# Kernel optimization log

Measured on AMD Instinct MI355X. Metric: run time of the kernel, lower is better.

Reference implementation:

```python
import jax, jax.numpy as jnp
import numpy as np

NEG = -9999.0
PAD_IDX = 0
SOS_IDX = 47


def setup_inputs() -> dict:
    key = jax.random.key(0)
    k1, k2, k3 = jax.random.split(key, 3)
    B, T, S = 1024, 512, 48
    features = jax.random.normal(k1, (B, T, S), dtype=jnp.float32)
    states = jax.random.randint(k2, (B, T), 1, S - 1)  # avoid pad/sos as gold tags
    mask = jnp.ones((B, T), dtype=jnp.float32)
    # transition matrix ~ N(-1, 0.1) with CRF structural constraints (as in __init__)
    transition = -1.0 + 0.1 * jax.random.normal(k3, (S, S), dtype=jnp.float32)
    transition = transition.at[SOS_IDX, :].set(NEG)
    transition = transition.at[:, PAD_IDX].set(NEG)
    transition = transition.at[PAD_IDX, :].set(NEG)
    transition = transition.at[PAD_IDX, PAD_IDX].set(0.0)
    return {"features": features, "states": states, "mask": mask, "transition": transition}


def _numerator(features, states, mask, transition):
    # score of the gold path: sum_t mask_t * (emission_t + transition[y_t, y_{t-1}])
    B = states.shape[0]
    sos_col = jnp.full((B, 1), SOS_IDX, dtype=states.dtype)
    states_ext = jnp.concatenate([sos_col, states], axis=1)  # [B, T+1]
    emis = jnp.take_along_axis(features, states[..., None], axis=2)[..., 0]  # [B, T]
    trans = transition[states_ext[:, 1:], states_ext[:, :-1]]  # [B, T]
    return jnp.sum((emis + trans) * mask, axis=1)  # [B]


def _denominator(features, mask, transition):
    # CRF forward algorithm: log-partition via log-sum-exp scan over time
    B, T, S = features.shape
    init = jnp.full((B, S), NEG, dtype=features.dtype).at[:, SOS_IDX].set(0.0)

    def step(score, xs):
        emis_t, mask_t = xs  # [B, S], [B]
        # new[b, i] = lse_j( score[b, j] + emis[b, i] + transition[i, j] )
        new = jax.nn.logsumexp(
            score[:, None, :] + emis_t[:, :, None] + transition[None, :, :], axis=-1
        )
        m = mask_t[:, None]
        return new * m + score * (1.0 - m), None

    final, _ = jax.lax.scan(
        step, init, (jnp.swapaxes(features, 0, 1), jnp.swapaxes(mask, 0, 1))
    )
    return jax.nn.logsumexp(final, axis=-1)  # [B]


def reference(features, states, mask, transition):
    numer = _numerator(features, states, mask, transition)
    denom = _denominator(features, mask, transition)
    # per-sequence negative log-likelihood (denominator - numerator)
    return denom - numer
```

## Files before the change

### kernel.cpp

```cpp
#include <hip/hip_runtime.h>
#include <math.h>

#define B 1024
#define T 512
#define S 48
#define SOS 47

__device__ __forceinline__ float rdlane1(float v) {
    return __int_as_float(__builtin_amdgcn_readlane(__float_as_int(v), 1));
}

__global__ __launch_bounds__(64)
__attribute__((amdgpu_waves_per_eu(1, 1)))
void crf_fused(const float* __restrict__ feat,
               const int* __restrict__ states,
               const float* __restrict__ mask,
               const float* __restrict__ trans,
               float* __restrict__ out) {
    __shared__ __align__(16) float pbuf[2][64];
    __shared__ unsigned long long mbits[T / 64];
    const int b = blockIdx.x;
    const int lane = threadIdx.x;
    const int elane = (lane < S) ? lane : 0;
    const float* f_b = feat + (size_t)b * T * S;
    const float* m_b = mask + b * T;
    const int* st_b = states + b * T;

    float nsum = 0.f;
#pragma unroll
    for (int k2 = 0; k2 < T / 64; ++k2) {
        const int t = lane + k2 * 64;
        const int st = st_b[t];
        const int pv = (t == 0) ? SOS : st_b[t - 1];
        const float m = m_b[t];
        nsum += (f_b[t * S + st] + trans[st * S + pv]) * m;
        const unsigned long long bal = __ballot(m != 0.f);
        if (lane == 0) mbits[k2] = bal;
    }

    float expT[S];
    {
        const float4* t4 = (const float4*)(trans + elane * S);
#pragma unroll
        for (int j4 = 0; j4 < S / 4; ++j4) {
            const float4 tv = t4[j4];
            expT[4 * j4 + 0] = (lane < S) ? __expf(tv.x) : 0.f;
            expT[4 * j4 + 1] = (lane < S) ? __expf(tv.y) : 0.f;
            expT[4 * j4 + 2] = (lane < S) ? __expf(tv.z) : 0.f;
            expT[4 * j4 + 3] = (lane < S) ? __expf(tv.w) : 0.f;
        }
    }

    float q = (lane == SOS) ? 1.f : 0.f;
    float M = 0.f;
    float r_s = 1.f, l_s = 0.f;
    pbuf[0][lane] = q;

    float ering[2][8];
#pragma unroll
    for (int k = 0; k < 8; ++k)
        ering[0][k] = f_b[k * S + elane];

#pragma unroll 2
    for (int tb = 0; tb < T / 8; ++tb) {
        const int pb = tb & 1;
        const int tn = ((tb + 1) & (T / 8 - 1)) * 8;
#pragma unroll
        for (int k = 0; k < 8; ++k)
            ering[pb ^ 1][k] = f_b[(tn + k) * S + elane];
        const unsigned int mbyte =
            ((const volatile unsigned char*)mbits)[tb];
#pragma unroll
        for (int k = 0; k < 8; ++k) {
            const float emis = ering[pb][k];
            const float er = rdlane1(emis);
            const float F = __expf(emis - er) * r_s;
            const float4* qb = (const float4*)pbuf[k & 1];
            float ax = 0.f, ay = 0.f, az = 0.f, aw = 0.f;
#pragma unroll
            for (int j4 = 0; j4 < S / 4; ++j4) {
                const float4 pv4 = qb[j4];
                ax = fmaf(expT[4 * j4 + 0], pv4.x, ax);
                ay = fmaf(expT[4 * j4 + 1], pv4.y, ay);
                az = fmaf(expT[4 * j4 + 2], pv4.z, az);
                aw = fmaf(expT[4 * j4 + 3], pv4.w, aw);
            }
            const float d = (ax + ay) + (az + aw);
            const float qn = d * F;
            const bool live = ((mbyte >> k) & 1u) != 0u;
            q = live ? qn : q;
            pbuf[(k + 1) & 1][lane] = q;
            M = live ? (M + er + l_s) : M;
            const float dr = rdlane1(d);
            const float nl = __logf(dr);
            const float nr = __builtin_amdgcn_rcpf(dr);
            r_s = live ? nr : r_s;
            l_s = live ? nl : l_s;
        }
    }

    float ps = q;
#pragma unroll
    for (int off = 32; off > 0; off >>= 1) {
        ps += __shfl_xor(ps, off, 64);
        nsum += __shfl_xor(nsum, off, 64);
    }
    if (lane == 0) out[b] = M + __logf(ps) - nsum;
}

extern "C" void kernel_launch(void* const* d_in, const int* in_sizes, int n_in,
                              void* d_out, int out_size, void* d_ws, size_t ws_size,
                              hipStream_t stream) {
    const float* feat   = (const float*)d_in[0];
    const int*   states = (const int*)d_in[1];
    const float* mask   = (const float*)d_in[2];
    const float* trans  = (const float*)d_in[3];
    float* out = (float*)d_out;

    crf_fused<<<dim3(B), dim3(64), 0, stream>>>(feat, states, mask, trans, out);
}
```

Measured before the change: 286.7 us.

## Use fp16 dot2 for CRF recurrence and track normalizer via exponent bookkeeping

The exp-transition matrix and the per-step probability vector in LDS are stored as fp16, and the 48-term matvec uses v_dot2 fdot2 instructions, which halves both the FMA count and the LDS read bytes. Per-step normalization now divides by lane 1's value and accumulates the reciprocal scale as a float mantissa plus an integer exponent, so no log is needed per step. The loop unroll drops from 2 to 1. In exchange, fp16 precision risks accuracy loss in the log-partition over 512 steps.

Result: slower. 310.3 us (+8.2%).

```diff
diff --git a/kernel.cpp b/kernel.cpp
--- a/kernel.cpp
+++ b/kernel.cpp
@@ -5,6 +5,9 @@
 #define T 512
 #define S 48
 #define SOS 47
+
+typedef _Float16 half2v __attribute__((ext_vector_type(2)));
+typedef _Float16 half8v __attribute__((ext_vector_type(8)));
 
 __device__ __forceinline__ float rdlane1(float v) {
     return __int_as_float(__builtin_amdgcn_readlane(__float_as_int(v), 1));
@@ -17,7 +20,7 @@
                const float* __restrict__ mask,
                const float* __restrict__ trans,
                float* __restrict__ out) {
-    __shared__ __align__(16) float pbuf[2][64];
+    __shared__ __align__(16) _Float16 qbuf[2][64];
     __shared__ unsigned long long mbits[T / 64];
     const int b = blockIdx.x;
     const int lane = threadIdx.x;
@@ -38,64 +41,71 @@
         if (lane == 0) mbits[k2] = bal;
     }
 
-    float expT[S];
+    half2v eT[S / 2];
     {
         const float4* t4 = (const float4*)(trans + elane * S);
 #pragma unroll
         for (int j4 = 0; j4 < S / 4; ++j4) {
             const float4 tv = t4[j4];
-            expT[4 * j4 + 0] = (lane < S) ? __expf(tv.x) : 0.f;
-            expT[4 * j4 + 1] = (lane < S) ? __expf(tv.y) : 0.f;
-            expT[4 * j4 + 2] = (lane < S) ? __expf(tv.z) : 0.f;
-            expT[4 * j4 + 3] = (lane < S) ? __expf(tv.w) : 0.f;
+            const float e0 = (lane < S) ? __expf(tv.x) : 0.f;
+            const float e1 = (lane < S) ? __expf(tv.y) : 0.f;
+            const float e2 = (lane < S) ? __expf(tv.z) : 0.f;
+            const float e3 = (lane < S) ? __expf(tv.w) : 0.f;
+            eT[2 * j4 + 0] = half2v{(_Float16)e0, (_Float16)e1};
+            eT[2 * j4 + 1] = half2v{(_Float16)e2, (_Float16)e3};
         }
     }
 
     float q = (lane == SOS) ? 1.f : 0.f;
-    float M = 0.f;
-    float r_s = 1.f, l_s = 0.f;
-    pbuf[0][lane] = q;
+    qbuf[0][lane] = (_Float16)q;
+    float P = 1.f;
+    int cexp = 0;
 
     float ering[2][8];
 #pragma unroll
     for (int k = 0; k < 8; ++k)
         ering[0][k] = f_b[k * S + elane];
 
-#pragma unroll 2
+#pragma unroll 1
     for (int tb = 0; tb < T / 8; ++tb) {
-        const int pb = tb & 1;
+        const int pbk = tb & 1;
         const int tn = ((tb + 1) & (T / 8 - 1)) * 8;
 #pragma unroll
         for (int k = 0; k < 8; ++k)
-            ering[pb ^ 1][k] = f_b[(tn + k) * S + elane];
+            ering[pbk ^ 1][k] = f_b[(tn + k) * S + elane];
         const unsigned int mbyte =
             ((const volatile unsigned char*)mbits)[tb];
 #pragma unroll
         for (int k = 0; k < 8; ++k) {
-            const float emis = ering[pb][k];
-            const float er = rdlane1(emis);
-            const float F = __expf(emis - er) * r_s;
-            const float4* qb = (const float4*)pbuf[k & 1];
+            asm volatile("" ::: "memory");
+            const float E = __expf(ering[pbk][k]);
+            const half8v* qb = (const half8v*)&qbuf[k & 1][0];
             float ax = 0.f, ay = 0.f, az = 0.f, aw = 0.f;
 #pragma unroll
-            for (int j4 = 0; j4 < S / 4; ++j4) {
-                const float4 pv4 = qb[j4];
-                ax = fmaf(expT[4 * j4 + 0], pv4.x, ax);
-                ay = fmaf(expT[4 * j4 + 1], pv4.y, ay);
-                az = fmaf(expT[4 * j4 + 2], pv4.z, az);
-                aw = fmaf(expT[4 * j4 + 3], pv4.w, aw);
+            for (int c = 0; c < 6; ++c) {
+                const half8v h = qb[c];
+                const half2v p0 = __builtin_shufflevector(h, h, 0, 1);
+                const half2v p1 = __builtin_shufflevector(h, h, 2, 3);
+                const half2v p2 = __builtin_shufflevector(h, h, 4, 5);
+                const half2v p3 = __builtin_shufflevector(h, h, 6, 7);
+                ax = __builtin_amdgcn_fdot2(eT[4 * c + 0], p0, ax, false);
+                ay = __builtin_amdgcn_fdot2(eT[4 * c + 1], p1, ay, false);
+                az = __builtin_amdgcn_fdot2(eT[4 * c + 2], p2, az, false);
+                aw = __builtin_amdgcn_fdot2(eT[4 * c + 3], p3, aw, false);
             }
             const float d = (ax + ay) + (az + aw);
-            const float qn = d * F;
+            const float t = d * E;
+            const float t1 = rdlane1(t);
+            const float r = __builtin_amdgcn_rcpf(t1);
+            const float qn = t * r;
             const bool live = ((mbyte >> k) & 1u) != 0u;
             q = live ? qn : q;
-            pbuf[(k + 1) & 1][lane] = q;
-            M = live ? (M + er + l_s) : M;
-            const float dr = rdlane1(d);
-            const float nl = __logf(dr);
-            const float nr = __builtin_amdgcn_rcpf(dr);
-            r_s = live ? nr : r_s;
-            l_s = live ? nl : l_s;
+            qbuf[(k + 1) & 1][lane] = (_Float16)q;
+            const float f = live ? r : 1.f;
+            P *= f;
+            const int pbits = __float_as_int(P);
+            cexp += (pbits >> 23) - 127;
+            P = __int_as_float((pbits & 0x007FFFFF) | 0x3F800000);
         }
     }
 
@@ -105,7 +115,10 @@
         ps += __shfl_xor(ps, off, 64);
         nsum += __shfl_xor(nsum, off, 64);
     }
-    if (lane == 0) out[b] = M + __logf(ps) - nsum;
+    if (lane == 0) {
+        const float C = -((float)cexp * 0.69314718056f + __logf(P));
+        out[b] = C + __logf(ps) - nsum;
+    }
 }
 
 extern "C" void kernel_launch(void* const* d_in, const int* in_sizes, int n_in,
```
